# Kernel tuning notes

Measured on AMD Instinct MI355X. Metric: run time of the kernel, lower is better.

## Reference

```python
import jax, jax.numpy as jnp
import numpy as np

B, N, C = 2, 65536, 256
HEADS, DIM_HEAD, SLICE_NUM = 8, 64, 64
INNER = HEADS * DIM_HEAD


def setup_inputs() -> dict:
    key = jax.random.key(0)
    ks = jax.random.split(key, 7)
    s_in = 1.0 / np.sqrt(C)
    s_dh = 1.0 / np.sqrt(DIM_HEAD)
    return {
        "x": jax.random.normal(ks[0], (B, N, C), dtype=jnp.float32),
        "Wx": jax.random.uniform(ks[1], (C, INNER), jnp.float32, -s_in, s_in),
        "bx": jax.random.uniform(ks[2], (INNER,), jnp.float32, -s_in, s_in),
        "Wfx": jax.random.uniform(ks[3], (C, INNER), jnp.float32, -s_in, s_in),
        "bfx": jax.random.uniform(ks[4], (INNER,), jnp.float32, -s_in, s_in),
        "Wslice": jax.random.uniform(ks[5], (DIM_HEAD, SLICE_NUM), jnp.float32, -s_dh, s_dh),
        "bslice": jax.random.uniform(ks[6], (SLICE_NUM,), jnp.float32, -s_dh, s_dh),
        "temperature": jnp.ones((1, HEADS, 1, 1), dtype=jnp.float32) * 0.5,
    }


def reference(x, Wx, bx, Wfx, bfx, Wslice, bslice, temperature):
    b, n, _ = x.shape
    # Linear projections, split heads: (B, N, H*D) -> (B, H, N, D)
    px = (x @ Wx + bx).reshape(b, n, HEADS, DIM_HEAD).transpose(0, 2, 1, 3)
    fx = (x @ Wfx + bfx).reshape(b, n, HEADS, DIM_HEAD).transpose(0, 2, 1, 3)
    # Project onto slices: (B, H, N, S)
    slice_proj = px @ Wslice + bslice
    # Temperature-scaled softmax over slices
    temp = jnp.clip(temperature, 0.5, 5.0)
    slice_weights = jax.nn.softmax(slice_proj / temp, axis=-1)
    # Normalize by per-slice mass over tokens, then aggregate
    slice_norm = slice_weights.sum(axis=2)  # (B, H, S)
    normed = slice_weights / (slice_norm[:, :, None, :] + 0.01)
    slice_tokens = jnp.einsum("bhns,bhnd->bhsd", normed, fx)
    return slice_tokens
```

## Files before the change

kernel.cpp:

```cpp
#include <hip/hip_runtime.h>
#include <hip/hip_bf16.h>


typedef __attribute__((ext_vector_type(8))) short short8;
typedef __attribute__((ext_vector_type(4))) short short4v;
typedef __attribute__((ext_vector_type(4))) float float4v;
typedef __attribute__((ext_vector_type(2))) unsigned int uint2v;

#define WPITCH 264
#define MP 36

__device__ __forceinline__ unsigned short f2bf(float f) {
    union { float f; unsigned int u; } v; v.f = f;
    unsigned int r = (v.u + 0x7FFFu + ((v.u >> 16) & 1u)) >> 16;
    return (unsigned short)r;
}

__device__ __forceinline__ unsigned int pack2(float a, float b) {
    __hip_bfloat162 h = __float22bfloat162_rn(float2{a, b});
    union { __hip_bfloat162 h; unsigned int u; } cv; cv.h = h;
    return cv.u;
}

__global__ __launch_bounds__(256)
void msfe_xprep(const float* __restrict__ x, unsigned short* __restrict__ xf) {
    __shared__ unsigned short Xs[64 * WPITCH];
    const int blk = blockIdx.x;
    const int tid = threadIdx.x;
    const float4v* xg = (const float4v*)(x + (long)blk * 64 * 256);
    #pragma unroll
    for (int i = 0; i < 16; ++i) {
        float4v v = xg[tid + i * 256];
        int f = (tid + i * 256) * 4;
        int row = f >> 8, col = f & 255;
        unsigned int lo = pack2(v.x, v.y), hi = pack2(v.z, v.w);
        *(unsigned int*)(Xs + row * WPITCH + col)     = lo;
        *(unsigned int*)(Xs + row * WPITCH + col + 2) = hi;
    }
    __syncthreads();
    const int wv = tid >> 6, lane = tid & 63;
    const int quad = lane >> 4, l16 = lane & 15;
    const int chunkL = wv >> 1, tw = wv & 1;
    unsigned short* ob = xf + (((long)(blk * 2 + chunkL) * 2 + tw) * 4096) + (long)lane * 8;
    const int row0 = chunkL * 32 + tw * 16 + l16;
    #pragma unroll
    for (int ks = 0; ks < 8; ++ks) {
        short8 o = *(const short8*)(Xs + row0 * WPITCH + ks * 32 + quad * 8);
        *(short8*)(ob + ks * 512) = o;
    }
}

__global__ __launch_bounds__(256)
void msfe_prep4(const float* __restrict__ Wx, const float* __restrict__ bx,
                const float* __restrict__ Wfx,
                const float* __restrict__ Wslice, const float* __restrict__ bslice,
                unsigned short* __restrict__ WtF, float* __restrict__ bcv) {
    const int b = blockIdx.x, t = threadIdx.x;
    if (b < 256) {
        const int head = b >> 5, oct = b & 31;
        __shared__ float Wsl[64 * 65];
        __shared__ float WxS[8 * 64];
        __shared__ unsigned short stg[8 * 64];
        #pragma unroll
        for (int i = 0; i < 16; ++i) {
            int idx = i * 256 + t; int d = idx >> 6, s = idx & 63;
            Wsl[d * 65 + s] = Wslice[idx];
        }
        #pragma unroll
        for (int i = 0; i < 2; ++i) {
            int idx = i * 256 + t; int j = idx >> 6, d = idx & 63;
            WxS[j * 64 + d] = Wx[(long)(oct * 8 + j) * 512 + head * 64 + d];
        }
        __syncthreads();
        const int s = t & 63;
        #pragma unroll
        for (int rep = 0; rep < 2; ++rep) {
            int j = (t >> 6) + rep * 4;
            float a0 = 0.f, a1 = 0.f, a2 = 0.f, a3 = 0.f;
            #pragma unroll
            for (int d = 0; d < 64; d += 4) {
                a0 += WxS[j * 64 + d]     * Wsl[(d)     * 65 + s];
                a1 += WxS[j * 64 + d + 1] * Wsl[(d + 1) * 65 + s];
                a2 += WxS[j * 64 + d + 2] * Wsl[(d + 2) * 65 + s];
                a3 += WxS[j * 64 + d + 3] * Wsl[(d + 3) * 65 + s];
            }
            stg[j * 64 + s] = f2bf((a0 + a1) + (a2 + a3));
        }
        __syncthreads();
        if (t < 64) {
            int nt = t >> 4, l16 = t & 15;
            int ks = oct >> 2, quad = oct & 3;
            int lane = quad * 16 + l16;
            short8 o;
            #pragma unroll
            for (int j = 0; j < 8; ++j) o[j] = (short)stg[j * 64 + nt * 16 + l16];
            *(short8*)(WtF + ((((long)(0 * 8 + head) * 4 + nt) * 8 + ks) * 64 + lane) * 8) = o;
        }
    } else if (b < 320) {
        const int head = (b - 256) >> 3, ks = (b - 256) & 7;
        const int nt = t >> 6, lane = t & 63;
        const int quad = lane >> 4, l16 = lane & 15;
        short8 o;
        #pragma unroll
        for (int j = 0; j < 8; ++j)
            o[j] = (short)f2bf(Wfx[(long)(ks * 32 + quad * 8 + j) * 512 + head * 64 + nt * 16 + l16]);
        *(short8*)(WtF + ((((long)(1 * 8 + head) * 4 + nt) * 8 + ks) * 64 + lane) * 8) = o;
    } else {
        #pragma unroll
        for (int p = 0; p < 2; ++p) {
            int j = t + p * 256;
            int h = j >> 6, s = j & 63;
            float bsum = bslice[s];
            for (int d = 0; d < 64; ++d) bsum += bx[h * 64 + d] * Wslice[d * 64 + s];
            bcv[j] = bsum;
        }
    }
}

__global__ __launch_bounds__(256, 2)
void msfe_main5(const unsigned short* __restrict__ xf,
                const unsigned short* __restrict__ WtF,
                const float* __restrict__ bcv,
                const float* __restrict__ bfx,
                const float* __restrict__ temperature,
                float* __restrict__ Tg, float* __restrict__ ng) {
    __shared__ unsigned short wT[2][64 * MP];
    __shared__ unsigned short fT[2][64 * MP];

    const int tid  = threadIdx.x;
    const int lane = tid & 63;
    const int wv   = tid >> 6;
    const int quad = lane >> 4;
    const int l16  = lane & 15;

    const int bidx = blockIdx.x;
    const int tile = (bidx >> 6) * 8 + (bidx & 7);
    const int head = (bidx >> 3) & 7;
    const int batch = tile >> 7;

    const int proj = wv >> 1;
    const int tw   = wv & 1;

    short8 wfr[4][8];
    {
        const unsigned short* wb = WtF + (((long)(proj * 8 + head) * 4) * 8) * 512 + (long)lane * 8;
        #pragma unroll
        for (int nt = 0; nt < 4; ++nt)
            #pragma unroll
            for (int ks = 0; ks < 8; ++ks)
                wfr[nt][ks] = *(const short8*)(wb + (nt * 8 + ks) * 512);
    }
    #pragma unroll
    for (int nt = 0; nt < 4; ++nt)
        #pragma unroll
        for (int ks = 0; ks < 8; ++ks)
            asm volatile("" : "+a"(wfr[nt][ks]));

    float bias[4];
    #pragma unroll
    for (int nt = 0; nt < 4; ++nt)
        bias[nt] = (proj == 0 ? bcv : bfx)[head * 64 + nt * 16 + l16];
    float tmp = temperature[head];
    tmp = fminf(fmaxf(tmp, 0.5f), 5.0f);
    const float invt = 1.0f / tmp;

    float4v Tac[4];
    #pragma unroll
    for (int nt = 0; nt < 4; ++nt) Tac[nt] = (float4v){0.f, 0.f, 0.f, 0.f};
    float normAcc[4] = {0.f, 0.f, 0.f, 0.f};

    const unsigned short* xb = xf + (((long)tile * 16 * 2 + tw) * 4096) + (long)lane * 8;
    short8 afr[8];
    #pragma unroll
    for (int ks = 0; ks < 8; ++ks)
        afr[ks] = *(const short8*)(xb + ks * 512);

    for (int c = 0; c < 16; ++c) {
        const int wbuf = c & 1, rbuf = wbuf ^ 1;

        float4v acc[4];
        #pragma unroll
        for (int nt = 0; nt < 4; ++nt) acc[nt] = (float4v){0.f, 0.f, 0.f, 0.f};
        #pragma unroll
        for (int ks = 0; ks < 8; ++ks) {
            #pragma unroll
            for (int nt = 0; nt < 4; ++nt)
                acc[nt] = __builtin_amdgcn_mfma_f32_16x16x32_bf16(afr[ks], wfr[nt][ks], acc[nt], 0, 0, 0);
        }

        if (c < 15) {
            #pragma unroll
            for (int ks = 0; ks < 8; ++ks)
                afr[ks] = *(const short8*)(xb + (long)(c + 1) * 8192 + ks * 512);
        }

        if (c > 0) {
            short8 a = *(const short8*)(&wT[rbuf][(wv * 16 + l16) * MP + quad * 8]);
            #pragma unroll
            for (int nt = 0; nt < 4; ++nt) {
                short8 bf = *(const short8*)(&fT[rbuf][(nt * 16 + l16) * MP + quad * 8]);
                Tac[nt] = __builtin_amdgcn_mfma_f32_16x16x32_bf16(a, bf, Tac[nt], 0, 0, 0);
            }
        }

        if (proj == 0) {
            float e[4][4];
            #pragma unroll
            for (int nt = 0; nt < 4; ++nt)
                #pragma unroll
                for (int rr = 0; rr < 4; ++rr)
                    e[nt][rr] = __expf((acc[nt][rr] + bias[nt]) * invt);
            #pragma unroll
            for (int rr = 0; rr < 4; ++rr) {
                float s = e[0][rr] + e[1][rr] + e[2][rr] + e[3][rr];
                s += __shfl_xor(s, 1); s += __shfl_xor(s, 2);
                s += __shfl_xor(s, 4); s += __shfl_xor(s, 8);
                float inv = 1.0f / s;
                e[0][rr] *= inv; e[1][rr] *= inv; e[2][rr] *= inv; e[3][rr] *= inv;
            }
            #pragma unroll
            for (int nt = 0; nt < 4; ++nt) {
                normAcc[nt] += e[nt][0] + e[nt][1] + e[nt][2] + e[nt][3];
                uint2v p;
                p.x = pack2(e[nt][0], e[nt][1]);
                p.y = pack2(e[nt][2], e[nt][3]);
                *(uint2v*)(&wT[wbuf][(nt * 16 + l16) * MP + tw * 16 + quad * 4]) = p;
            }
        } else {
            #pragma unroll
            for (int nt = 0; nt < 4; ++nt) {
                uint2v p;
                p.x = pack2(acc[nt][0] + bias[nt], acc[nt][1] + bias[nt]);
                p.y = pack2(acc[nt][2] + bias[nt], acc[nt][3] + bias[nt]);
                *(uint2v*)(&fT[wbuf][(nt * 16 + l16) * MP + tw * 16 + quad * 4]) = p;
            }
        }

        __syncthreads();
    }

    {
        short8 a = *(const short8*)(&wT[1][(wv * 16 + l16) * MP + quad * 8]);
        #pragma unroll
        for (int nt = 0; nt < 4; ++nt) {
            short8 bf = *(const short8*)(&fT[1][(nt * 16 + l16) * MP + quad * 8]);
            Tac[nt] = __builtin_amdgcn_mfma_f32_16x16x32_bf16(a, bf, Tac[nt], 0, 0, 0);
        }
    }

    const int basehs = (batch * 8 + head) * 64;
    #pragma unroll
    for (int nt = 0; nt < 4; ++nt) {
        #pragma unroll
        for (int rr = 0; rr < 4; ++rr) {
            int s = wv * 16 + quad * 4 + rr;
            int d = nt * 16 + l16;
            atomicAdd(&Tg[(basehs + s) * 64 + d], Tac[nt][rr]);
        }
    }
    if (proj == 0) {
        #pragma unroll
        for (int nt = 0; nt < 4; ++nt) {
            float v = normAcc[nt];
            v += __shfl_xor(v, 16);
            v += __shfl_xor(v, 32);
            if (quad == 0) atomicAdd(&ng[basehs + nt * 16 + l16], v);
        }
    }
}

__global__ void msfe_final(const float* __restrict__ Tg, const float* __restrict__ ng,
                           float* __restrict__ out) {
    int i = blockIdx.x * 256 + threadIdx.x;
    out[i] = Tg[i] / (ng[i >> 6] + 0.01f);
}

extern "C" void kernel_launch(void* const* d_in, const int* in_sizes, int n_in,
                              void* d_out, int out_size, void* d_ws, size_t ws_size,
                              hipStream_t stream) {
    const float* x       = (const float*)d_in[0];
    const float* Wx      = (const float*)d_in[1];
    const float* bx      = (const float*)d_in[2];
    const float* Wfx     = (const float*)d_in[3];
    const float* bfx     = (const float*)d_in[4];
    const float* Wslice  = (const float*)d_in[5];
    const float* bslice  = (const float*)d_in[6];
    const float* temp    = (const float*)d_in[7];

    char* ws = (char*)d_ws;
    unsigned short* xf  = (unsigned short*)ws;
    unsigned short* WtF = (unsigned short*)(ws + 67108864);
    float* bc = (float*)(ws + 67633152);
    float* Tg = (float*)(ws + 67635200);
    float* ng = (float*)(ws + 67897344);

    hipMemsetAsync(Tg, 0, 262144 + 4096, stream);
    msfe_prep4<<<321, 256, 0, stream>>>(Wx, bx, Wfx, Wslice, bslice, WtF, bc);
    msfe_xprep<<<2048, 256, 0, stream>>>(x, xf);
    msfe_main5<<<2048, 256, 0, stream>>>(xf, WtF, bc, bfx, temp, Tg, ng);
    msfe_final<<<256, 256, 0, stream>>>(Tg, ng, (float*)d_out);
}
```

Before: 336.5 us.

## Fuse x fp32-to-bf16 conversion into main kernel via double-buffered LDS staging

Removes the separate xprep kernel, which converted x to bf16 in an MFMA-friendly layout in a workspace buffer. The main kernel now loads fp32 x directly and packs it to bf16 into a double-buffered LDS tile. The next chunk's global loads are issued while the current chunk's MFMAs run. This avoids writing and re-reading the intermediate bf16 copy and saves a launch. In exchange, each of the 8 per-head blocks now reads fp32 rows, twice the bytes of bf16, and LDS use per block grows, which may strain occupancy at two blocks per CU.

```diff
diff --git a/kernel.cpp b/kernel.cpp
--- a/kernel.cpp
+++ b/kernel.cpp
@@ -7,8 +7,8 @@
 typedef __attribute__((ext_vector_type(4))) float float4v;
 typedef __attribute__((ext_vector_type(2))) unsigned int uint2v;
 
-#define WPITCH 264
 #define MP 36
+#define XP 264
 
 __device__ __forceinline__ unsigned short f2bf(float f) {
     union { float f; unsigned int u; } v; v.f = f;
@@ -20,34 +20,6 @@
     __hip_bfloat162 h = __float22bfloat162_rn(float2{a, b});
     union { __hip_bfloat162 h; unsigned int u; } cv; cv.h = h;
     return cv.u;
-}
-
-__global__ __launch_bounds__(256)
-void msfe_xprep(const float* __restrict__ x, unsigned short* __restrict__ xf) {
-    __shared__ unsigned short Xs[64 * WPITCH];
-    const int blk = blockIdx.x;
-    const int tid = threadIdx.x;
-    const float4v* xg = (const float4v*)(x + (long)blk * 64 * 256);
-    #pragma unroll
-    for (int i = 0; i < 16; ++i) {
-        float4v v = xg[tid + i * 256];
-        int f = (tid + i * 256) * 4;
-        int row = f >> 8, col = f & 255;
-        unsigned int lo = pack2(v.x, v.y), hi = pack2(v.z, v.w);
-        *(unsigned int*)(Xs + row * WPITCH + col)     = lo;
-        *(unsigned int*)(Xs + row * WPITCH + col + 2) = hi;
-    }
-    __syncthreads();
-    const int wv = tid >> 6, lane = tid & 63;
-    const int quad = lane >> 4, l16 = lane & 15;
-    const int chunkL = wv >> 1, tw = wv & 1;
-    unsigned short* ob = xf + (((long)(blk * 2 + chunkL) * 2 + tw) * 4096) + (long)lane * 8;
-    const int row0 = chunkL * 32 + tw * 16 + l16;
-    #pragma unroll
-    for (int ks = 0; ks < 8; ++ks) {
-        short8 o = *(const short8*)(Xs + row0 * WPITCH + ks * 32 + quad * 8);
-        *(short8*)(ob + ks * 512) = o;
-    }
 }
 
 __global__ __launch_bounds__(256)
@@ -118,7 +90,7 @@
 }
 
 __global__ __launch_bounds__(256, 2)
-void msfe_main5(const unsigned short* __restrict__ xf,
+void msfe_main6(const float* __restrict__ x,
                 const unsigned short* __restrict__ WtF,
                 const float* __restrict__ bcv,
                 const float* __restrict__ bfx,
@@ -126,6 +98,7 @@
                 float* __restrict__ Tg, float* __restrict__ ng) {
     __shared__ unsigned short wT[2][64 * MP];
     __shared__ unsigned short fT[2][64 * MP];
+    __shared__ __align__(16) unsigned short XS[2][32 * XP];
 
     const int tid  = threadIdx.x;
     const int lane = tid & 63;
@@ -169,15 +142,30 @@
     for (int nt = 0; nt < 4; ++nt) Tac[nt] = (float4v){0.f, 0.f, 0.f, 0.f};
     float normAcc[4] = {0.f, 0.f, 0.f, 0.f};
 
-    const unsigned short* xb = xf + (((long)tile * 16 * 2 + tw) * 4096) + (long)lane * 8;
-    short8 afr[8];
-    #pragma unroll
-    for (int ks = 0; ks < 8; ++ks)
-        afr[ks] = *(const short8*)(xb + ks * 512);
+    const float4v* xg4 = (const float4v*)(x + (long)tile * 512 * 256);
+
+    {
+        float4v xs[8];
+        #pragma unroll
+        for (int i = 0; i < 8; ++i) xs[i] = xg4[i * 256 + tid];
+        #pragma unroll
+        for (int i = 0; i < 8; ++i) {
+            uint2v p;
+            p.x = pack2(xs[i].x, xs[i].y);
+            p.y = pack2(xs[i].z, xs[i].w);
+            *(uint2v*)(&XS[0][(i * 4 + wv) * XP + lane * 4]) = p;
+        }
+    }
+    __syncthreads();
 
     for (int c = 0; c < 16; ++c) {
         const int wbuf = c & 1, rbuf = wbuf ^ 1;
 
+        short8 afr[8];
+        #pragma unroll
+        for (int ks = 0; ks < 8; ++ks)
+            afr[ks] = *(const short8*)(&XS[wbuf][(tw * 16 + l16) * XP + ks * 32 + quad * 8]);
+
         float4v acc[4];
         #pragma unroll
         for (int nt = 0; nt < 4; ++nt) acc[nt] = (float4v){0.f, 0.f, 0.f, 0.f};
@@ -188,10 +176,11 @@
                 acc[nt] = __builtin_amdgcn_mfma_f32_16x16x32_bf16(afr[ks], wfr[nt][ks], acc[nt], 0, 0, 0);
         }
 
+        float4v xst[8];
         if (c < 15) {
             #pragma unroll
-            for (int ks = 0; ks < 8; ++ks)
-                afr[ks] = *(const short8*)(xb + (long)(c + 1) * 8192 + ks * 512);
+            for (int i = 0; i < 8; ++i)
+                xst[i] = xg4[(c + 1) * 2048 + i * 256 + tid];
         }
 
         if (c > 0) {
@@ -233,6 +222,16 @@
                 p.x = pack2(acc[nt][0] + bias[nt], acc[nt][1] + bias[nt]);
                 p.y = pack2(acc[nt][2] + bias[nt], acc[nt][3] + bias[nt]);
                 *(uint2v*)(&fT[wbuf][(nt * 16 + l16) * MP + tw * 16 + quad * 4]) = p;
+            }
+        }
+
+        if (c < 15) {
+            #pragma unroll
+            for (int i = 0; i < 8; ++i) {
+                uint2v p;
+                p.x = pack2(xst[i].x, xst[i].y);
+                p.y = pack2(xst[i].z, xst[i].w);
+                *(uint2v*)(&XS[rbuf][(i * 4 + wv) * XP + lane * 4]) = p;
             }
         }
 
@@ -288,7 +287,6 @@
     const float* temp    = (const float*)d_in[7];
 
     char* ws = (char*)d_ws;
-    unsigned short* xf  = (unsigned short*)ws;
     unsigned short* WtF = (unsigned short*)(ws + 67108864);
     float* bc = (float*)(ws + 67633152);
     float* Tg = (float*)(ws + 67635200);
@@ -296,7 +294,6 @@
 
     hipMemsetAsync(Tg, 0, 262144 + 4096, stream);
     msfe_prep4<<<321, 256, 0, stream>>>(Wx, bx, Wfx, Wslice, bslice, WtF, bc);
-    msfe_xprep<<<2048, 256, 0, stream>>>(x, xf);
-    msfe_main5<<<2048, 256, 0, stream>>>(xf, WtF, bc, bfx, temp, Tg, ng);
+    msfe_main6<<<2048, 256, 0, stream>>>(x, WtF, bc, bfx, temp, Tg, ng);
     msfe_final<<<256, 256, 0, stream>>>(Tg, ng, (float*)d_out);
 }
```

After: 309.5 us. 1.09x faster.
